# Kernel optimization log

Hardware: AMD Instinct MI355X
Metric: run time of the kernel (lower is better)

Reference implementation:

```python
import jax, jax.numpy as jnp
import numpy as np

N = 50000      # nodes
E = 800000     # edges (before self-loops)
IN = 128       # input_dim
HID = 64       # hidden_dim
EMB = 32       # embedding_dim
HEADS = 4
NEG_SLOPE = 0.2
BN_EPS = 1e-5


def setup_inputs() -> dict:
    key = jax.random.key(0)
    ks = jax.random.split(key, 20)
    s = 0.1
    x = jax.random.normal(ks[0], (N, IN), jnp.float32)
    edge_index = jax.random.randint(ks[1], (2, E), 0, N, dtype=jnp.int64)
    # GAT layer 0: 128 -> 64, 4 heads, concat
    W0 = jax.random.normal(ks[2], (IN, HEADS * HID), jnp.float32) * s
    a_src0 = jax.random.normal(ks[3], (HEADS, HID), jnp.float32) * s
    a_dst0 = jax.random.normal(ks[4], (HEADS, HID), jnp.float32) * s
    b0 = jax.random.normal(ks[5], (HEADS * HID,), jnp.float32) * s
    # BatchNorm1d(256) in eval mode (running stats)
    bn_gamma = jax.random.uniform(ks[6], (HEADS * HID,), jnp.float32, 0.5, 1.5)
    bn_beta = jax.random.normal(ks[7], (HEADS * HID,), jnp.float32) * s
    bn_mean = jax.random.normal(ks[8], (HEADS * HID,), jnp.float32) * s
    bn_var = jax.random.uniform(ks[9], (HEADS * HID,), jnp.float32, 0.5, 1.5)
    # GAT layer 1: 256 -> 32, 1 head, mean (concat=False)
    W1 = jax.random.normal(ks[10], (HEADS * HID, EMB), jnp.float32) * s
    a_src1 = jax.random.normal(ks[11], (1, EMB), jnp.float32) * s
    a_dst1 = jax.random.normal(ks[12], (1, EMB), jnp.float32) * s
    b1 = jax.random.normal(ks[13], (EMB,), jnp.float32) * s
    # prediction head: Linear(32,64) -> ReLU -> Linear(64,1)
    head_W1 = jax.random.normal(ks[14], (EMB, HID), jnp.float32) * s
    head_b1 = jax.random.normal(ks[15], (HID,), jnp.float32) * s
    head_W2 = jax.random.normal(ks[16], (HID, 1), jnp.float32) * s
    head_b2 = jax.random.normal(ks[17], (1,), jnp.float32) * s
    return dict(x=x, edge_index=edge_index, W0=W0, a_src0=a_src0, a_dst0=a_dst0, b0=b0,
                bn_gamma=bn_gamma, bn_beta=bn_beta, bn_mean=bn_mean, bn_var=bn_var,
                W1=W1, a_src1=a_src1, a_dst1=a_dst1, b1=b1,
                head_W1=head_W1, head_b1=head_b1, head_W2=head_W2, head_b2=head_b2)


def _gat_conv(x, src, dst, W, a_src, a_dst, bias, heads, out_c, concat):
    # PyG GATConv (eval mode, dropout off, self-loops already in src/dst)
    n = x.shape[0]
    h = (x @ W).reshape(n, heads, out_c)                # [N,H,C]
    alpha_s = jnp.sum(h * a_src, axis=-1)               # [N,H]
    alpha_d = jnp.sum(h * a_dst, axis=-1)               # [N,H]
    e = alpha_s[src] + alpha_d[dst]                      # [Etot,H]
    e = jnp.where(e > 0, e, NEG_SLOPE * e)               # leaky_relu
    m = jax.ops.segment_max(e, dst, num_segments=n)      # softmax over incoming edges
    e = jnp.exp(e - m[dst])
    denom = jax.ops.segment_sum(e, dst, num_segments=n)
    alpha = e / denom[dst]                               # [Etot,H]; self-loops ensure denom>0
    out = jax.ops.segment_sum(h[src] * alpha[:, :, None], dst, num_segments=n)  # [N,H,C]
    out = out.reshape(n, heads * out_c) if concat else out.mean(axis=1)
    return out + bias


def reference(x, edge_index, W0, a_src0, a_dst0, b0,
              bn_gamma, bn_beta, bn_mean, bn_var,
              W1, a_src1, a_dst1, b1,
              head_W1, head_b1, head_W2, head_b2):
    n = x.shape[0]
    loops = jnp.arange(n, dtype=edge_index.dtype)
    src = jnp.concatenate([edge_index[0], loops])
    dst = jnp.concatenate([edge_index[1], loops])

    h = _gat_conv(x, src, dst, W0, a_src0, a_dst0, b0, HEADS, HID, True)   # [N,256]
    h = (h - bn_mean) * (bn_gamma / jnp.sqrt(bn_var + BN_EPS)) + bn_beta   # BN eval
    h = jax.nn.relu(h)                                                      # dropout off (eval)
    node_embeddings = _gat_conv(h, src, dst, W1, a_src1, a_dst1, b1, 1, EMB, False)  # [N,32]

    graph_embedding = jnp.mean(node_embeddings, axis=0, keepdims=True)      # [1,32]
    hid = jax.nn.relu(graph_embedding @ head_W1 + head_b1)
    predictions = hid @ head_W2 + head_b2                                    # [1,1]
    return node_embeddings, predictions
```

## Files before the change

kernel.cpp:

```cpp
#include <hip/hip_runtime.h>


#define NEG_SLOPE 0.2f
#define BN_EPS 1e-5f
#define LOG2E 1.4426950408889634f

typedef __attribute__((ext_vector_type(8))) short bf16x8;
typedef __attribute__((ext_vector_type(4))) float f32x4;

__device__ __forceinline__ float bf2f(unsigned short u) {
  return __uint_as_float((unsigned)u << 16);
}
__device__ __forceinline__ unsigned short f2bf(float f) {
  unsigned u = __float_as_uint(f);
  u += 0x7fff + ((u >> 16) & 1);
  return (unsigned short)(u >> 16);
}

__global__ __launch_bounds__(256) void hist_swz_kernel(
    const int* __restrict__ dsts, int* __restrict__ deg, int E, int N,
    int histBlocks, const float* __restrict__ W0, const float* __restrict__ W1,
    unsigned short* __restrict__ w0sw, unsigned short* __restrict__ w1sw) {
  const int b = blockIdx.x;
  if (b < histBlocks) {
    int e = b * 256 + threadIdx.x;
    if (e >= E + N) return;
    int d = (e < E) ? dsts[e] : e - E;
    atomicAdd(&deg[d], 1);
  } else {
    int o = (b - histBlocks) * 256 + threadIdx.x;
    if (o < 32768) {
      int j = o & 7, l = (o >> 3) & 63, ks = (o >> 9) & 3,
          ci = (o >> 11) & 3, h = (o >> 13) & 3;
      int row = ks * 32 + (l >> 4) * 8 + j;
      int col = h * 64 + ci * 16 + (l & 15);
      w0sw[o] = f2bf(W0[row * 256 + col]);
    } else if (o < 40960) {
      int o2 = o - 32768;
      int j = o2 & 7, l = (o2 >> 3) & 63, ks = (o2 >> 9) & 7, ci = (o2 >> 12) & 1;
      int row = ks * 32 + (l >> 4) * 8 + j;
      int col = ci * 16 + (l & 15);
      w1sw[o2] = f2bf(W1[row * 32 + col]);
    }
  }
}

__global__ __launch_bounds__(256) void gemm0_mfma_kernel(
    const float* __restrict__ x, const unsigned short* __restrict__ w0sw,
    const float* __restrict__ a_src0, const float* __restrict__ a_dst0,
    unsigned short* __restrict__ h0bf, float* __restrict__ as0,
    float* __restrict__ ad0, int M) {
  __shared__ unsigned short Asw[16 * 64 * 8];
  const int t = threadIdx.x;
  const int lane = t & 63;
  const int h = t >> 6;
  const int row0 = blockIdx.x * 64;

  #pragma unroll
  for (int i = 0; i < 8; ++i) {
    int q = t + 256 * i;
    int r = q >> 5, c4 = q & 31;
    int gr = row0 + r;
    float4 v = make_float4(0.f, 0.f, 0.f, 0.f);
    if (gr < M) v = *reinterpret_cast<const float4*>(&x[(size_t)gr * 128 + c4 * 4]);
    int ks = c4 >> 3;
    int lane_hi = (c4 >> 1) & 3;
    int j0 = (c4 & 1) * 4;
    int slot = (r >> 4) * 4 + ks;
    int dlane = (r & 15) + 16 * lane_hi;
    ushort4 o;
    o.x = f2bf(v.x); o.y = f2bf(v.y); o.z = f2bf(v.z); o.w = f2bf(v.w);
    *reinterpret_cast<ushort4*>(&Asw[(slot * 64 + dlane) * 8 + j0]) = o;
  }
  __syncthreads();

  f32x4 acc[4][4] = {};
  const bf16x8* wp = reinterpret_cast<const bf16x8*>(w0sw);
  #pragma unroll
  for (int ks = 0; ks < 4; ++ks) {
    bf16x8 bfrag[4];
    #pragma unroll
    for (int ci = 0; ci < 4; ++ci)
      bfrag[ci] = wp[(h * 16 + ci * 4 + ks) * 64 + lane];
    #pragma unroll
    for (int ri = 0; ri < 4; ++ri) {
      bf16x8 af = *reinterpret_cast<const bf16x8*>(&Asw[((ri * 4 + ks) * 64 + lane) * 8]);
      #pragma unroll
      for (int ci = 0; ci < 4; ++ci)
        acc[ri][ci] = __builtin_amdgcn_mfma_f32_16x16x32_bf16(af, bfrag[ci], acc[ri][ci], 0, 0, 0);
    }
  }

  float av[4], dv[4];
  #pragma unroll
  for (int ci = 0; ci < 4; ++ci) {
    av[ci] = a_src0[h * 64 + ci * 16 + (lane & 15)];
    dv[ci] = a_dst0[h * 64 + ci * 16 + (lane & 15)];
  }
  const int mrow = (lane >> 4) * 4;
  #pragma unroll
  for (int ri = 0; ri < 4; ++ri) {
    #pragma unroll
    for (int r = 0; r < 4; ++r) {
      int gr = row0 + ri * 16 + mrow + r;
      float ps = acc[ri][0][r] * av[0] + acc[ri][1][r] * av[1] +
                 acc[ri][2][r] * av[2] + acc[ri][3][r] * av[3];
      float pd = acc[ri][0][r] * dv[0] + acc[ri][1][r] * dv[1] +
                 acc[ri][2][r] * dv[2] + acc[ri][3][r] * dv[3];
      #pragma unroll
      for (int off = 1; off < 16; off <<= 1) {
        ps += __shfl_xor(ps, off);
        pd += __shfl_xor(pd, off);
      }
      if (gr < M) {
        #pragma unroll
        for (int ci = 0; ci < 4; ++ci)
          h0bf[(size_t)gr * 256 + h * 64 + ci * 16 + (lane & 15)] = f2bf(acc[ri][ci][r]);
        if ((lane & 15) == 0) { as0[gr * 4 + h] = ps * LOG2E; ad0[gr * 4 + h] = pd * LOG2E; }
      }
    }
  }
}

__global__ __launch_bounds__(256) void scan_block_kernel(
    const int* __restrict__ deg, int* __restrict__ excl,
    int* __restrict__ bsum, int N) {
  __shared__ int tmp[256];
  int i = blockIdx.x * 256 + threadIdx.x;
  int v = (i < N) ? deg[i] : 0;
  tmp[threadIdx.x] = v;
  __syncthreads();
  #pragma unroll
  for (int off = 1; off < 256; off <<= 1) {
    int t = (threadIdx.x >= off) ? tmp[threadIdx.x - off] : 0;
    __syncthreads();
    tmp[threadIdx.x] += t;
    __syncthreads();
  }
  if (i < N) excl[i] = tmp[threadIdx.x] - v;
  if (threadIdx.x == 255) bsum[blockIdx.x] = tmp[255];
}

__global__ __launch_bounds__(256) void scan_add_kernel(
    int* __restrict__ rowptr, const int* __restrict__ bsum,
    int* __restrict__ cursor, int N, int Etot) {
  __shared__ int wred[4];
  const int t = threadIdx.x;
  int v = (t < blockIdx.x) ? bsum[t] : 0;
  #pragma unroll
  for (int off = 32; off >= 1; off >>= 1) v += __shfl_xor(v, off);
  if ((t & 63) == 0) wred[t >> 6] = v;
  __syncthreads();
  const int prefix = wred[0] + wred[1] + wred[2] + wred[3];
  int i = blockIdx.x * 256 + t;
  if (i < N) {
    int r = rowptr[i] + prefix;
    rowptr[i] = r;
    cursor[i] = r;
  }
  if (i == 0) rowptr[N] = Etot;
}

__global__ __launch_bounds__(256) void scatter_kernel(
    const int* __restrict__ srcs, const int* __restrict__ dsts,
    int* __restrict__ cursor, int* __restrict__ csr_src, int E, int N) {
  int e = blockIdx.x * 256 + threadIdx.x;
  if (e >= E + N) return;
  int s, d;
  if (e < E) { s = srcs[e]; d = dsts[e]; } else { s = d = e - E; }
  int pos = atomicAdd(&cursor[d], 1);
  csr_src[pos] = s;
}

__global__ __launch_bounds__(256) void agg0_kernel(
    const int* __restrict__ rowptr, const int* __restrict__ csr_src,
    const unsigned short* __restrict__ h0bf, const float* __restrict__ as0,
    const float* __restrict__ ad0, const float* __restrict__ b0,
    const float* __restrict__ gamma, const float* __restrict__ beta,
    const float* __restrict__ mean, const float* __restrict__ var,
    const unsigned short* __restrict__ w1sw,
    const float* __restrict__ a_src1, const float* __restrict__ a_dst1,
    unsigned short* __restrict__ h1bf, float* __restrict__ as1,
    float* __restrict__ ad1, int N) {
  __shared__ float wlds[4][64];
  __shared__ unsigned short Asw2[8 * 64 * 8];
  const int lane = threadIdx.x & 63;
  const int wid = threadIdx.x >> 6;
  const int n = blockIdx.x * 4 + wid;
  const bool valid = n < N;
  const int h = lane >> 4;
  const int eidx = lane & 15;
  const int bb = lane & 48;

  if (valid) {
    const int beg = rowptr[n], end = rowptr[n + 1];
    const float adv = ad0[n * 4 + h];
    float4 acc = make_float4(0.f, 0.f, 0.f, 0.f);
    float wsum = 0.f;

    int i = beg;
    int ne = (end - i < 16) ? (end - i) : 16;
    int src = csr_src[i + (eidx < ne ? eidx : ne - 1)];

    #pragma unroll 1
    while (i < end) {
      const int srccur = src;
      const int necur = ne;

      const int s0 = __builtin_amdgcn_readlane(srccur, 0);
      const int s1 = __builtin_amdgcn_readlane(srccur, 1);
      const int s2 = __builtin_amdgcn_readlane(srccur, 2);
      const int s3 = __builtin_amdgcn_readlane(srccur, 3);
      const int s4 = __builtin_amdgcn_readlane(srccur, 4);
      const int s5 = __builtin_amdgcn_readlane(srccur, 5);
      const int s6 = __builtin_amdgcn_readlane(srccur, 6);
      const int s7 = __builtin_amdgcn_readlane(srccur, 7);
      ushort4 v0 = *reinterpret_cast<const ushort4*>(&(h0bf + (size_t)s0 * 256)[lane * 4]);
      ushort4 v1 = *reinterpret_cast<const ushort4*>(&(h0bf + (size_t)s1 * 256)[lane * 4]);
      ushort4 v2 = *reinterpret_cast<const ushort4*>(&(h0bf + (size_t)s2 * 256)[lane * 4]);
      ushort4 v3 = *reinterpret_cast<const ushort4*>(&(h0bf + (size_t)s3 * 256)[lane * 4]);
      ushort4 v4 = *reinterpret_cast<const ushort4*>(&(h0bf + (size_t)s4 * 256)[lane * 4]);
      ushort4 v5 = *reinterpret_cast<const ushort4*>(&(h0bf + (size_t)s5 * 256)[lane * 4]);
      ushort4 v6 = *reinterpret_cast<const ushort4*>(&(h0bf + (size_t)s6 * 256)[lane * 4]);
      ushort4 v7 = *reinterpret_cast<const ushort4*>(&(h0bf + (size_t)s7 * 256)[lane * 4]);

      i += 16;
      if (i < end) {
        ne = (end - i < 16) ? (end - i) : 16;
        src = csr_src[i + (eidx < ne ? eidx : ne - 1)];
      }

      float xx = as0[(unsigned)(srccur * 4 + h)] + adv;
      xx = fmaxf(xx, NEG_SLOPE * xx);
      float wl = (eidx < necur) ? exp2f(xx) : 0.f;
      wsum += wl;
      wlds[wid][lane] = wl;

      {
        const float w0 = wlds[wid][bb + 0], w1 = wlds[wid][bb + 1];
        const float w2 = wlds[wid][bb + 2], w3 = wlds[wid][bb + 3];
        const float w4 = wlds[wid][bb + 4], w5 = wlds[wid][bb + 5];
        const float w6 = wlds[wid][bb + 6], w7 = wlds[wid][bb + 7];
        acc.x += ((w0 * bf2f(v0.x) + w1 * bf2f(v1.x)) + (w2 * bf2f(v2.x) + w3 * bf2f(v3.x))) +
                 ((w4 * bf2f(v4.x) + w5 * bf2f(v5.x)) + (w6 * bf2f(v6.x) + w7 * bf2f(v7.x)));
        acc.y += ((w0 * bf2f(v0.y) + w1 * bf2f(v1.y)) + (w2 * bf2f(v2.y) + w3 * bf2f(v3.y))) +
                 ((w4 * bf2f(v4.y) + w5 * bf2f(v5.y)) + (w6 * bf2f(v6.y) + w7 * bf2f(v7.y)));
        acc.z += ((w0 * bf2f(v0.z) + w1 * bf2f(v1.z)) + (w2 * bf2f(v2.z) + w3 * bf2f(v3.z))) +
                 ((w4 * bf2f(v4.z) + w5 * bf2f(v5.z)) + (w6 * bf2f(v6.z) + w7 * bf2f(v7.z)));
        acc.w += ((w0 * bf2f(v0.w) + w1 * bf2f(v1.w)) + (w2 * bf2f(v2.w) + w3 * bf2f(v3.w))) +
                 ((w4 * bf2f(v4.w) + w5 * bf2f(v5.w)) + (w6 * bf2f(v6.w) + w7 * bf2f(v7.w)));
      }
      if (necur > 8) {
        const int t0 = __builtin_amdgcn_readlane(srccur, 8);
        const int t1 = __builtin_amdgcn_readlane(srccur, 9);
        const int t2 = __builtin_amdgcn_readlane(srccur, 10);
        const int t3 = __builtin_amdgcn_readlane(srccur, 11);
        const int t4 = __builtin_amdgcn_readlane(srccur, 12);
        const int t5 = __builtin_amdgcn_readlane(srccur, 13);
        const int t6 = __builtin_amdgcn_readlane(srccur, 14);
        const int t7 = __builtin_amdgcn_readlane(srccur, 15);
        ushort4 u0 = *reinterpret_cast<const ushort4*>(&(h0bf + (size_t)t0 * 256)[lane * 4]);
        ushort4 u1 = *reinterpret_cast<const ushort4*>(&(h0bf + (size_t)t1 * 256)[lane * 4]);
        ushort4 u2 = *reinterpret_cast<const ushort4*>(&(h0bf + (size_t)t2 * 256)[lane * 4]);
        ushort4 u3 = *reinterpret_cast<const ushort4*>(&(h0bf + (size_t)t3 * 256)[lane * 4]);
        ushort4 u4 = *reinterpret_cast<const ushort4*>(&(h0bf + (size_t)t4 * 256)[lane * 4]);
        ushort4 u5 = *reinterpret_cast<const ushort4*>(&(h0bf + (size_t)t5 * 256)[lane * 4]);
        ushort4 u6 = *reinterpret_cast<const ushort4*>(&(h0bf + (size_t)t6 * 256)[lane * 4]);
        ushort4 u7 = *reinterpret_cast<const ushort4*>(&(h0bf + (size_t)t7 * 256)[lane * 4]);
        const float w0 = wlds[wid][bb + 8],  w1 = wlds[wid][bb + 9];
        const float w2 = wlds[wid][bb + 10], w3 = wlds[wid][bb + 11];
        const float w4 = wlds[wid][bb + 12], w5 = wlds[wid][bb + 13];
        const float w6 = wlds[wid][bb + 14], w7 = wlds[wid][bb + 15];
        acc.x += ((w0 * bf2f(u0.x) + w1 * bf2f(u1.x)) + (w2 * bf2f(u2.x) + w3 * bf2f(u3.x))) +
                 ((w4 * bf2f(u4.x) + w5 * bf2f(u5.x)) + (w6 * bf2f(u6.x) + w7 * bf2f(u7.x)));
        acc.y += ((w0 * bf2f(u0.y) + w1 * bf2f(u1.y)) + (w2 * bf2f(u2.y) + w3 * bf2f(u3.y))) +
                 ((w4 * bf2f(u4.y) + w5 * bf2f(u5.y)) + (w6 * bf2f(u6.y) + w7 * bf2f(u7.y)));
        acc.z += ((w0 * bf2f(u0.z) + w1 * bf2f(u1.z)) + (w2 * bf2f(u2.z) + w3 * bf2f(u3.z))) +
                 ((w4 * bf2f(u4.z) + w5 * bf2f(u5.z)) + (w6 * bf2f(u6.z) + w7 * bf2f(u7.z)));
        acc.w += ((w0 * bf2f(u0.w) + w1 * bf2f(u1.w)) + (w2 * bf2f(u2.w) + w3 * bf2f(u3.w))) +
                 ((w4 * bf2f(u4.w) + w5 * bf2f(u5.w)) + (w6 * bf2f(u6.w) + w7 * bf2f(u7.w)));
      }
    }

    #pragma unroll
    for (int off = 1; off < 16; off <<= 1) wsum += __shfl_xor(wsum, off);

    const float inv = 1.0f / wsum;
    const int j = lane * 4;
    float4 bbv = *reinterpret_cast<const float4*>(&b0[j]);
    float4 mu = *reinterpret_cast<const float4*>(&mean[j]);
    float4 gg = *reinterpret_cast<const float4*>(&gamma[j]);
    float4 vv = *reinterpret_cast<const float4*>(&var[j]);
    float4 be = *reinterpret_cast<const float4*>(&beta[j]);
    float4 o;
    o.x = (acc.x * inv + bbv.x - mu.x) * (gg.x * rsqrtf(vv.x + BN_EPS)) + be.x;
    o.y = (acc.y * inv + bbv.y - mu.y) * (gg.y * rsqrtf(vv.y + BN_EPS)) + be.y;
    o.z = (acc.z * inv + bbv.z - mu.z) * (gg.z * rsqrtf(vv.z + BN_EPS)) + be.z;
    o.w = (acc.w * inv + bbv.w - mu.w) * (gg.w * rsqrtf(vv.w + BN_EPS)) + be.w;
    ushort4 ob;
    ob.x = f2bf(fmaxf(o.x, 0.f)); ob.y = f2bf(fmaxf(o.y, 0.f));
    ob.z = f2bf(fmaxf(o.z, 0.f)); ob.w = f2bf(fmaxf(o.w, 0.f));
    const int ks = lane >> 3;
    const int lane_hi = (lane >> 1) & 3;
    const int j0 = (lane & 1) * 4;
    const int dlane = wid + 16 * lane_hi;
    *reinterpret_cast<ushort4*>(&Asw2[(ks * 64 + dlane) * 8 + j0]) = ob;
  }
  __syncthreads();

  if (wid == 0) {
    const bf16x8* bp = reinterpret_cast<const bf16x8*>(w1sw);
    f32x4 c0 = {}, c1 = {};
    #pragma unroll
    for (int ks = 0; ks < 8; ++ks) {
      bf16x8 af = *reinterpret_cast<const bf16x8*>(&Asw2[(ks * 64 + lane) * 8]);
      c0 = __builtin_amdgcn_mfma_f32_16x16x32_bf16(af, bp[(0 * 8 + ks) * 64 + lane], c0, 0, 0, 0);
      c1 = __builtin_amdgcn_mfma_f32_16x16x32_bf16(af, bp[(1 * 8 + ks) * 64 + lane], c1, 0, 0, 0);
    }
    const float av0 = a_src1[lane & 15], av1 = a_src1[16 + (lane & 15)];
    const float dv0 = a_dst1[lane & 15], dv1 = a_dst1[16 + (lane & 15)];
    const int rowgrp = lane >> 4;
    #pragma unroll
    for (int r = 0; r < 4; ++r) {
      float ps = c0[r] * av0 + c1[r] * av1;
      float pd = c0[r] * dv0 + c1[r] * dv1;
      #pragma unroll
      for (int off = 1; off < 16; off <<= 1) {
        ps += __shfl_xor(ps, off);
        pd += __shfl_xor(pd, off);
      }
      const int gn = blockIdx.x * 4 + r;
      if (rowgrp == 0 && gn < N) {
        h1bf[(size_t)gn * 32 + (lane & 15)]      = f2bf(c0[r]);
        h1bf[(size_t)gn * 32 + 16 + (lane & 15)] = f2bf(c1[r]);
        if ((lane & 15) == 0) { as1[gn] = ps * LOG2E; ad1[gn] = pd * LOG2E; }
      }
    }
  }
}

__global__ __launch_bounds__(256) void agg1_kernel(
    const int* __restrict__ rowptr, const int* __restrict__ csr_src,
    const unsigned short* __restrict__ h1bf, const float* __restrict__ as1,
    const float* __restrict__ ad1, const float* __restrict__ b1,
    float* __restrict__ out, float* __restrict__ gsum16, int N) {
  __shared__ float wslab[4][16];
  __shared__ int sslab[4][16];
  __shared__ float gred[4][32];
  const int t = threadIdx.x;
  const int lane = t & 63;
  const int wid = t >> 6;
  const int n = blockIdx.x * 4 + wid;
  const bool valid = n < N;
  const int c = lane & 31;
  const int half = lane >> 5;
  float val = 0.f;

  if (valid) {
    const int beg = rowptr[n], end = rowptr[n + 1];
    const float adv = ad1[n];
    float acc = 0.f, wsum = 0.f;

    for (int i = beg; i < end; i += 16) {
      int ne = end - i; if (ne > 16) ne = 16;
      if (lane < 16) {
        const int idx = lane < ne ? lane : ne - 1;
        const int s = csr_src[i + idx];
        const float x = as1[s] + adv;
        const float wl = (lane < ne) ? exp2f(fmaxf(x, NEG_SLOPE * x)) : 0.f;
        wslab[wid][lane] = wl;
        sslab[wid][lane] = s;
        wsum += wl;
      }
      for (int e = 0; e < ne; e += 8) {
        const int i0 = e + half, i1 = e + 2 + half, i2 = e + 4 + half, i3 = e + 6 + half;
        const int s0 = sslab[wid][i0], s1 = sslab[wid][i1],
                  s2 = sslab[wid][i2], s3 = sslab[wid][i3];
        const float w0 = wslab[wid][i0], w1 = wslab[wid][i1],
                    w2 = wslab[wid][i2], w3 = wslab[wid][i3];
        const unsigned short u0 = h1bf[(size_t)s0 * 32 + c];
        const unsigned short u1 = h1bf[(size_t)s1 * 32 + c];
        const unsigned short u2 = h1bf[(size_t)s2 * 32 + c];
        const unsigned short u3 = h1bf[(size_t)s3 * 32 + c];
        acc += (w0 * bf2f(u0) + w1 * bf2f(u1)) + (w2 * bf2f(u2) + w3 * bf2f(u3));
      }
    }
    #pragma unroll
    for (int off = 1; off < 16; off <<= 1) wsum += __shfl_xor(wsum, off);
    wsum = __shfl(wsum, lane & 15);
    acc += __shfl_xor(acc, 32);
    if (half == 0) {
      val = acc / wsum + b1[c];
      out[(size_t)n * 32 + c] = val;
    }
  }

  if (half == 0) gred[wid][c] = val;
  __syncthreads();
  if (t < 32) {
    float v = gred[0][t] + gred[1][t] + gred[2][t] + gred[3][t];
    atomicAdd(&gsum16[(blockIdx.x & 15) * 32 + t], v);
  }
}

__global__ void pred_kernel(
    const float* __restrict__ gsum16, const float* __restrict__ hW1,
    const float* __restrict__ hb1, const float* __restrict__ hW2,
    const float* __restrict__ hb2, float* __restrict__ out, int N) {
  int j = threadIdx.x;
  float invN = 1.0f / (float)N;
  float acc = hb1[j];
  #pragma unroll
  for (int c = 0; c < 32; ++c) {
    float gv = 0.f;
    #pragma unroll
    for (int r = 0; r < 16; ++r) gv += gsum16[r * 32 + c];
    acc += (gv * invN) * hW1[c * 64 + j];
  }
  acc = fmaxf(acc, 0.f);
  float v = acc * hW2[j];
  #pragma unroll
  for (int off = 1; off < 64; off <<= 1) v += __shfl_xor(v, off);
  if (j == 0) out[(size_t)N * 32] = v + hb2[0];
}

extern "C" void kernel_launch(void* const* d_in, const int* in_sizes, int n_in,
                              void* d_out, int out_size, void* d_ws, size_t ws_size,
                              hipStream_t stream) {
  const float* x       = (const float*)d_in[0];
  const int*   ei      = (const int*)d_in[1];
  const float* W0      = (const float*)d_in[2];
  const float* a_src0  = (const float*)d_in[3];
  const float* a_dst0  = (const float*)d_in[4];
  const float* b0      = (const float*)d_in[5];
  const float* bn_g    = (const float*)d_in[6];
  const float* bn_b    = (const float*)d_in[7];
  const float* bn_m    = (const float*)d_in[8];
  const float* bn_v    = (const float*)d_in[9];
  const float* W1      = (const float*)d_in[10];
  const float* a_src1  = (const float*)d_in[11];
  const float* a_dst1  = (const float*)d_in[12];
  const float* b1      = (const float*)d_in[13];
  const float* hW1     = (const float*)d_in[14];
  const float* hb1     = (const float*)d_in[15];
  const float* hW2     = (const float*)d_in[16];
  const float* hb2     = (const float*)d_in[17];

  const int N = in_sizes[0] / 128;
  const int E = in_sizes[1] / 2;
  const int Etot = E + N;
  const int* srcs = ei;
  const int* dsts = ei + E;
  const int NB = (N + 255) / 256;

  float* out = (float*)d_out;

  float* ws = (float*)d_ws;
  size_t off = 0;
  unsigned short* h0bf   = (unsigned short*)(ws + off); off += (size_t)N * 128;
  unsigned short* h1bf   = (unsigned short*)(ws + off); off += (size_t)N * 16;
  unsigned short* w0sw   = (unsigned short*)(ws + off); off += 16384;
  unsigned short* w1sw   = (unsigned short*)(ws + off); off += 4096;
  float* as0    = ws + off; off += (size_t)N * 4;
  float* ad0    = ws + off; off += (size_t)N * 4;
  float* as1    = ws + off; off += (size_t)N;
  float* ad1    = ws + off; off += (size_t)N;
  int* rowptr   = (int*)(ws + off); off += (size_t)N + 1;
  int* cursor   = (int*)(ws + off); off += (size_t)N;
  int* bsum     = (int*)(ws + off); off += 256;
  int* csr_src  = (int*)(ws + off); off += (size_t)Etot;
  size_t zoff = off;
  int* deg      = (int*)(ws + off); off += (size_t)N;
  float* gsum16 = ws + off; off += 512;

  hipMemsetAsync(ws + zoff, 0, (off - zoff) * sizeof(float), stream);

  auto cdiv = [](long a, long b) { return (int)((a + b - 1) / b); };

  const int histBlocks = cdiv(Etot, 256);
  hist_swz_kernel<<<histBlocks + 160, 256, 0, stream>>>(
      dsts, deg, E, N, histBlocks, W0, W1, w0sw, w1sw);
  scan_block_kernel<<<NB, 256, 0, stream>>>(deg, rowptr, bsum, N);
  scan_add_kernel<<<NB, 256, 0, stream>>>(rowptr, bsum, cursor, N, Etot);
  scatter_kernel<<<cdiv(Etot, 256), 256, 0, stream>>>(srcs, dsts, cursor, csr_src, E, N);

  gemm0_mfma_kernel<<<cdiv(N, 64), 256, 0, stream>>>(
      x, w0sw, a_src0, a_dst0, h0bf, as0, ad0, N);
  agg0_kernel<<<cdiv(N, 4), 256, 0, stream>>>(
      rowptr, csr_src, h0bf, as0, ad0, b0, bn_g, bn_b, bn_m, bn_v,
      w1sw, a_src1, a_dst1, h1bf, as1, ad1, N);

  agg1_kernel<<<cdiv(N, 4), 256, 0, stream>>>(rowptr, csr_src, h1bf, as1, ad1,
                                              b1, out, gsum16, N);

  pred_kernel<<<1, 64, 0, stream>>>(gsum16, hW1, hb1, hW2, hb2, out, N);
}
```

Measured before the change: 236.6 us.

## Process nodes in degree-sorted order in aggregation kernels for load balance

Builds a degree histogram during the scan, prefix-sums it, and counting-sorts node ids by in-degree into an order array. agg0 and agg1 then map each wave to order[idx] instead of the raw node index, so waves within a block handle similar-degree nodes. This is meant to cut intra-block imbalance and tail effects from Poisson degree variation. It adds an extra kernel launch, atomics and an indirection, and it scatters output writes, which hurts locality on the dst side and in the agg0 MFMA writeback.

```diff
diff --git a/kernel.cpp b/kernel.cpp
--- a/kernel.cpp
+++ b/kernel.cpp
@@ -124,10 +124,11 @@
 
 __global__ __launch_bounds__(256) void scan_block_kernel(
     const int* __restrict__ deg, int* __restrict__ excl,
-    int* __restrict__ bsum, int N) {
+    int* __restrict__ bsum, int* __restrict__ dhist, int N) {
   __shared__ int tmp[256];
   int i = blockIdx.x * 256 + threadIdx.x;
   int v = (i < N) ? deg[i] : 0;
+  if (i < N) atomicAdd(&dhist[v > 255 ? 255 : v], 1);
   tmp[threadIdx.x] = v;
   __syncthreads();
   #pragma unroll
@@ -161,19 +162,49 @@
   if (i == 0) rowptr[N] = Etot;
 }
 
+__global__ __launch_bounds__(256) void dscan_kernel(
+    const int* __restrict__ dhist, int* __restrict__ dcursor) {
+  __shared__ int tmp[256];
+  const int t = threadIdx.x;
+  int v = dhist[t];
+  tmp[t] = v;
+  __syncthreads();
+  #pragma unroll
+  for (int off = 1; off < 256; off <<= 1) {
+    int u = (t >= off) ? tmp[t - off] : 0;
+    __syncthreads();
+    tmp[t] += u;
+    __syncthreads();
+  }
+  dcursor[t] = tmp[t] - v;
+}
+
 __global__ __launch_bounds__(256) void scatter_kernel(
     const int* __restrict__ srcs, const int* __restrict__ dsts,
-    int* __restrict__ cursor, int* __restrict__ csr_src, int E, int N) {
-  int e = blockIdx.x * 256 + threadIdx.x;
-  if (e >= E + N) return;
-  int s, d;
-  if (e < E) { s = srcs[e]; d = dsts[e]; } else { s = d = e - E; }
-  int pos = atomicAdd(&cursor[d], 1);
-  csr_src[pos] = s;
+    int* __restrict__ cursor, int* __restrict__ csr_src, int E, int N,
+    int edgeBlocks, const int* __restrict__ deg, int* __restrict__ dcursor,
+    int* __restrict__ order) {
+  const int b = blockIdx.x;
+  if (b < edgeBlocks) {
+    int e = b * 256 + threadIdx.x;
+    if (e >= E + N) return;
+    int s, d;
+    if (e < E) { s = srcs[e]; d = dsts[e]; } else { s = d = e - E; }
+    int pos = atomicAdd(&cursor[d], 1);
+    csr_src[pos] = s;
+  } else {
+    int i = (b - edgeBlocks) * 256 + threadIdx.x;
+    if (i < N) {
+      int dv = deg[i];
+      int pos = atomicAdd(&dcursor[dv > 255 ? 255 : dv], 1);
+      order[pos] = i;
+    }
+  }
 }
 
 __global__ __launch_bounds__(256) void agg0_kernel(
     const int* __restrict__ rowptr, const int* __restrict__ csr_src,
+    const int* __restrict__ order,
     const unsigned short* __restrict__ h0bf, const float* __restrict__ as0,
     const float* __restrict__ ad0, const float* __restrict__ b0,
     const float* __restrict__ gamma, const float* __restrict__ beta,
@@ -186,8 +217,9 @@
   __shared__ unsigned short Asw2[8 * 64 * 8];
   const int lane = threadIdx.x & 63;
   const int wid = threadIdx.x >> 6;
-  const int n = blockIdx.x * 4 + wid;
-  const bool valid = n < N;
+  const int idx = blockIdx.x * 4 + wid;
+  const bool valid = idx < N;
+  const int n = valid ? order[idx] : 0;
   const int h = lane >> 4;
   const int eidx = lane & 15;
   const int bb = lane & 48;
@@ -329,8 +361,9 @@
         ps += __shfl_xor(ps, off);
         pd += __shfl_xor(pd, off);
       }
-      const int gn = blockIdx.x * 4 + r;
-      if (rowgrp == 0 && gn < N) {
+      const int gidx = blockIdx.x * 4 + r;
+      if (rowgrp == 0 && gidx < N) {
+        const int gn = order[gidx];
         h1bf[(size_t)gn * 32 + (lane & 15)]      = f2bf(c0[r]);
         h1bf[(size_t)gn * 32 + 16 + (lane & 15)] = f2bf(c1[r]);
         if ((lane & 15) == 0) { as1[gn] = ps * LOG2E; ad1[gn] = pd * LOG2E; }
@@ -341,6 +374,7 @@
 
 __global__ __launch_bounds__(256) void agg1_kernel(
     const int* __restrict__ rowptr, const int* __restrict__ csr_src,
+    const int* __restrict__ order,
     const unsigned short* __restrict__ h1bf, const float* __restrict__ as1,
     const float* __restrict__ ad1, const float* __restrict__ b1,
     float* __restrict__ out, float* __restrict__ gsum16, int N) {
@@ -350,8 +384,9 @@
   const int t = threadIdx.x;
   const int lane = t & 63;
   const int wid = t >> 6;
-  const int n = blockIdx.x * 4 + wid;
-  const bool valid = n < N;
+  const int idx = blockIdx.x * 4 + wid;
+  const bool valid = idx < N;
+  const int n = valid ? order[idx] : 0;
   const int c = lane & 31;
   const int half = lane >> 5;
   float val = 0.f;
@@ -364,8 +399,8 @@
     for (int i = beg; i < end; i += 16) {
       int ne = end - i; if (ne > 16) ne = 16;
       if (lane < 16) {
-        const int idx = lane < ne ? lane : ne - 1;
-        const int s = csr_src[i + idx];
+        const int idx2 = lane < ne ? lane : ne - 1;
+        const int s = csr_src[i + idx2];
         const float x = as1[s] + adv;
         const float wl = (lane < ne) ? exp2f(fmaxf(x, NEG_SLOPE * x)) : 0.f;
         wslab[wid][lane] = wl;
@@ -469,8 +504,11 @@
   int* cursor   = (int*)(ws + off); off += (size_t)N;
   int* bsum     = (int*)(ws + off); off += 256;
   int* csr_src  = (int*)(ws + off); off += (size_t)Etot;
+  int* order    = (int*)(ws + off); off += (size_t)N;
+  int* dcursor  = (int*)(ws + off); off += 256;
   size_t zoff = off;
   int* deg      = (int*)(ws + off); off += (size_t)N;
+  int* dhist    = (int*)(ws + off); off += 256;
   float* gsum16 = ws + off; off += 512;
 
   hipMemsetAsync(ws + zoff, 0, (off - zoff) * sizeof(float), stream);
@@ -480,18 +518,21 @@
   const int histBlocks = cdiv(Etot, 256);
   hist_swz_kernel<<<histBlocks + 160, 256, 0, stream>>>(
       dsts, deg, E, N, histBlocks, W0, W1, w0sw, w1sw);
-  scan_block_kernel<<<NB, 256, 0, stream>>>(deg, rowptr, bsum, N);
+  scan_block_kernel<<<NB, 256, 0, stream>>>(deg, rowptr, bsum, dhist, N);
   scan_add_kernel<<<NB, 256, 0, stream>>>(rowptr, bsum, cursor, N, Etot);
-  scatter_kernel<<<cdiv(Etot, 256), 256, 0, stream>>>(srcs, dsts, cursor, csr_src, E, N);
+  dscan_kernel<<<1, 256, 0, stream>>>(dhist, dcursor);
+  const int edgeBlocks = cdiv(Etot, 256);
+  scatter_kernel<<<edgeBlocks + NB, 256, 0, stream>>>(
+      srcs, dsts, cursor, csr_src, E, N, edgeBlocks, deg, dcursor, order);
 
   gemm0_mfma_kernel<<<cdiv(N, 64), 256, 0, stream>>>(
       x, w0sw, a_src0, a_dst0, h0bf, as0, ad0, N);
   agg0_kernel<<<cdiv(N, 4), 256, 0, stream>>>(
-      rowptr, csr_src, h0bf, as0, ad0, b0, bn_g, bn_b, bn_m, bn_v,
+      rowptr, csr_src, order, h0bf, as0, ad0, b0, bn_g, bn_b, bn_m, bn_v,
       w1sw, a_src1, a_dst1, h1bf, as1, ad1, N);
 
-  agg1_kernel<<<cdiv(N, 4), 256, 0, stream>>>(rowptr, csr_src, h1bf, as1, ad1,
-                                              b1, out, gsum16, N);
+  agg1_kernel<<<cdiv(N, 4), 256, 0, stream>>>(rowptr, csr_src, order, h1bf,
+                                              as1, ad1, b1, out, gsum16, N);
 
   pred_kernel<<<1, 64, 0, stream>>>(gsum16, hW1, hb1, hW2, hb2, out, N);
 }
```

After: 499.2 us. +111.0%, slower.
